# Performance work log

Measured on AMD Instinct MI355X. Metric: run time of the kernel, lower is better.

The kernel has to match this reference:

```python
import jax, jax.numpy as jnp
import numpy as np

RANK = 16
ALPHA = 16.0
SCALING = ALPHA / RANK
N_ADAPTERS = 8


def setup_inputs() -> dict:
    key = jax.random.key(0)
    k_x, k_a, k_b, k_id = jax.random.split(key, 4)
    b, n, d_in, d_out = 8, 1024, 2048, 2048
    x = jax.random.normal(k_x, (b, n, d_in), dtype=jnp.float32)
    A = jax.random.normal(k_a, (N_ADAPTERS, d_out, RANK), dtype=jnp.float32) * 0.02
    B = jax.random.normal(k_b, (N_ADAPTERS, RANK, d_in), dtype=jnp.float32)
    adapter_ids = jax.random.randint(k_id, (b,), 0, N_ADAPTERS, dtype=jnp.int32)
    return {"x": x, "A": A, "B": B, "adapter_ids": adapter_ids}


def reference(x, A, B, adapter_ids):
    # Bx: [b, n, a, r] = einsum over in_features
    Bx = jnp.einsum('bni,ari->bnar', x, B)
    # result: [b, n, a, o]
    result = jnp.einsum('bnar,aor->bnao', Bx, A)
    # per-sample adapter gather: out[b, n, o] = result[b, n, adapter_ids[b], :]
    bidx = jnp.arange(x.shape[0])
    out = result[bidx, :, adapter_ids, :]  # [b, n, o]
    return out * SCALING  # dropout p=0.0 is identity
```

## Files before the change

kernel.cpp:

```cpp
#include <hip/hip_runtime.h>

#define D_IN   2048
#define D_OUT  2048
#define N_TOK  1024
#define N_B    8
#define RANK   16
#define TPB    8

__device__ __forceinline__ float dot4(float4 a, float4 b) {
    return a.x * b.x + a.y * b.y + a.z * b.z + a.w * b.w;
}

template <int CTRL>
__device__ __forceinline__ float dpp_add(float v) {
    int s = __builtin_amdgcn_update_dpp(0, __float_as_int(v), CTRL, 0xF, 0xF, true);
    return v + __int_as_float(s);
}

__device__ __forceinline__ float wave_sum(float v) {
    v = dpp_add<0xB1>(v);
    v = dpp_add<0x4E>(v);
    v = dpp_add<0x124>(v);
    v = dpp_add<0x128>(v);
    v += __shfl_xor(v, 16, 64);
    v += __shfl_xor(v, 32, 64);
    return v;
}

__global__ __launch_bounds__(256, 2)
void lora_fused_v4(const float* __restrict__ x,
                   const float* __restrict__ A,
                   const float* __restrict__ B,
                   const int* __restrict__ ids,
                   float* __restrict__ out) {
    __shared__ __align__(16) float bxs[TPB][RANK];

    const int b    = blockIdx.y;
    const int tok0 = blockIdx.x * TPB;
    const int aid  = ids[b];
    const int tid  = threadIdx.x;
    const int wave = tid >> 6;
    const int lane = tid & 63;

    const float* __restrict__ xb = x + ((size_t)b * N_TOK + tok0 + wave * 2) * D_IN;
    const float* __restrict__ Ba = B + (size_t)aid * RANK * D_IN;
    const float* __restrict__ Aa = A + (size_t)aid * D_OUT * RANK;
    float* __restrict__ ob = out + ((size_t)b * N_TOK + tok0) * D_OUT;

    float acc0[RANK], acc1[RANK];
    #pragma unroll
    for (int r = 0; r < RANK; ++r) { acc0[r] = 0.f; acc1[r] = 0.f; }

    #pragma unroll
    for (int chunk = 0; chunk < 8; ++chunk) {
        const int ib = chunk * 256 + lane * 4;
        const float4 xv0 = *reinterpret_cast<const float4*>(&xb[ib]);
        const float4 xv1 = *reinterpret_cast<const float4*>(&xb[D_IN + ib]);
        #pragma unroll
        for (int g = 0; g < 2; ++g) {
            float4 Bv[8];
            #pragma unroll
            for (int r = 0; r < 8; ++r)
                Bv[r] = *reinterpret_cast<const float4*>(&Ba[(size_t)(g * 8 + r) * D_IN + ib]);
            #pragma unroll
            for (int r = 0; r < 8; ++r) {
                acc0[g * 8 + r] += dot4(xv0, Bv[r]);
                acc1[g * 8 + r] += dot4(xv1, Bv[r]);
            }
        }
    }

    #pragma unroll
    for (int r = 0; r < RANK; ++r) {
        acc0[r] = wave_sum(acc0[r]);
        acc1[r] = wave_sum(acc1[r]);
    }

    if (lane == 0) {
        const int t0 = wave * 2;
        *reinterpret_cast<float4*>(&bxs[t0][0])      = make_float4(acc0[0],  acc0[1],  acc0[2],  acc0[3]);
        *reinterpret_cast<float4*>(&bxs[t0][4])      = make_float4(acc0[4],  acc0[5],  acc0[6],  acc0[7]);
        *reinterpret_cast<float4*>(&bxs[t0][8])      = make_float4(acc0[8],  acc0[9],  acc0[10], acc0[11]);
        *reinterpret_cast<float4*>(&bxs[t0][12])     = make_float4(acc0[12], acc0[13], acc0[14], acc0[15]);
        *reinterpret_cast<float4*>(&bxs[t0 + 1][0])  = make_float4(acc1[0],  acc1[1],  acc1[2],  acc1[3]);
        *reinterpret_cast<float4*>(&bxs[t0 + 1][4])  = make_float4(acc1[4],  acc1[5],  acc1[6],  acc1[7]);
        *reinterpret_cast<float4*>(&bxs[t0 + 1][8])  = make_float4(acc1[8],  acc1[9],  acc1[10], acc1[11]);
        *reinterpret_cast<float4*>(&bxs[t0 + 1][12]) = make_float4(acc1[12], acc1[13], acc1[14], acc1[15]);
    }
    __syncthreads();

    #pragma unroll
    for (int half = 0; half < 2; ++half) {
        const int o0 = half * 1024 + tid * 4;
        float4 Ar[4][4];
        #pragma unroll
        for (int j = 0; j < 4; ++j)
            #pragma unroll
            for (int q = 0; q < 4; ++q)
                Ar[j][q] = *reinterpret_cast<const float4*>(&Aa[(size_t)(o0 + j) * RANK + q * 4]);

        #pragma unroll
        for (int t = 0; t < TPB; ++t) {
            const float4 p0 = *reinterpret_cast<const float4*>(&bxs[t][0]);
            const float4 p1 = *reinterpret_cast<const float4*>(&bxs[t][4]);
            const float4 p2 = *reinterpret_cast<const float4*>(&bxs[t][8]);
            const float4 p3 = *reinterpret_cast<const float4*>(&bxs[t][12]);
            float4 res;
            res.x = dot4(Ar[0][0], p0) + dot4(Ar[0][1], p1) + dot4(Ar[0][2], p2) + dot4(Ar[0][3], p3);
            res.y = dot4(Ar[1][0], p0) + dot4(Ar[1][1], p1) + dot4(Ar[1][2], p2) + dot4(Ar[1][3], p3);
            res.z = dot4(Ar[2][0], p0) + dot4(Ar[2][1], p1) + dot4(Ar[2][2], p2) + dot4(Ar[2][3], p3);
            res.w = dot4(Ar[3][0], p0) + dot4(Ar[3][1], p1) + dot4(Ar[3][2], p2) + dot4(Ar[3][3], p3);
            *reinterpret_cast<float4*>(&ob[(size_t)t * D_OUT + o0]) = res;
        }
    }
}

extern "C" void kernel_launch(void* const* d_in, const int* in_sizes, int n_in,
                              void* d_out, int out_size, void* d_ws, size_t ws_size,
                              hipStream_t stream) {
    const float* x   = (const float*)d_in[0];
    const float* A   = (const float*)d_in[1];
    const float* B   = (const float*)d_in[2];
    const int*   ids = (const int*)d_in[3];
    float* out = (float*)d_out;

    dim3 grid(N_TOK / TPB, N_B);
    lora_fused_v4<<<grid, 256, 0, stream>>>(x, A, B, ids, out);
}
```

Baseline: 148.5 us.

## Split LoRA into split-K Bx kernel and separate output projection kernel

Replaces the fused single kernel with two launches. The first computes partial Bx products, with the input dimension split in two, and writes them to a workspace buffer. The second sums the two partials and applies the A projection, split across two output halves per block. This raises the number of blocks for both phases and shrinks per-thread register pressure, at the cost of an extra launch and a global-memory round trip for the small intermediate.

```diff
diff --git a/kernel.cpp b/kernel.cpp
--- a/kernel.cpp
+++ b/kernel.cpp
@@ -5,10 +5,15 @@
 #define N_TOK  1024
 #define N_B    8
 #define RANK   16
-#define TPB    8
+#define KSPLIT 2
+#define KHALF  (D_IN / KSPLIT)
 
 __device__ __forceinline__ float dot4(float4 a, float4 b) {
     return a.x * b.x + a.y * b.y + a.z * b.z + a.w * b.w;
+}
+
+__device__ __forceinline__ float4 f4add(float4 a, float4 b) {
+    return make_float4(a.x + b.x, a.y + b.y, a.z + b.z, a.w + b.w);
 }
 
 template <int CTRL>
@@ -27,45 +32,42 @@
     return v;
 }
 
+
 __global__ __launch_bounds__(256, 2)
-void lora_fused_v4(const float* __restrict__ x,
-                   const float* __restrict__ A,
-                   const float* __restrict__ B,
-                   const int* __restrict__ ids,
-                   float* __restrict__ out) {
-    __shared__ __align__(16) float bxs[TPB][RANK];
+void lora_bx(const float* __restrict__ x,
+             const float* __restrict__ B,
+             const int* __restrict__ ids,
+             float* __restrict__ W) {
+    const int tile = blockIdx.x;
+    const int ks   = blockIdx.y;
+    const int b    = blockIdx.z;
+    const int aid  = ids[b];
+    const int wave = (int)(threadIdx.x >> 6);
+    const int lane = (int)(threadIdx.x & 63);
+    const int t0   = tile * 8 + wave * 2;
 
-    const int b    = blockIdx.y;
-    const int tok0 = blockIdx.x * TPB;
-    const int aid  = ids[b];
-    const int tid  = threadIdx.x;
-    const int wave = tid >> 6;
-    const int lane = tid & 63;
-
-    const float* __restrict__ xb = x + ((size_t)b * N_TOK + tok0 + wave * 2) * D_IN;
-    const float* __restrict__ Ba = B + (size_t)aid * RANK * D_IN;
-    const float* __restrict__ Aa = A + (size_t)aid * D_OUT * RANK;
-    float* __restrict__ ob = out + ((size_t)b * N_TOK + tok0) * D_OUT;
+    const float* __restrict__ xb = x + ((size_t)b * N_TOK + t0) * D_IN + ks * KHALF;
+    const float* __restrict__ Ba = B + (size_t)aid * RANK * D_IN + ks * KHALF;
 
     float acc0[RANK], acc1[RANK];
     #pragma unroll
     for (int r = 0; r < RANK; ++r) { acc0[r] = 0.f; acc1[r] = 0.f; }
 
     #pragma unroll
-    for (int chunk = 0; chunk < 8; ++chunk) {
+    for (int chunk = 0; chunk < KHALF / 256; ++chunk) {
         const int ib = chunk * 256 + lane * 4;
         const float4 xv0 = *reinterpret_cast<const float4*>(&xb[ib]);
         const float4 xv1 = *reinterpret_cast<const float4*>(&xb[D_IN + ib]);
         #pragma unroll
-        for (int g = 0; g < 2; ++g) {
-            float4 Bv[8];
+        for (int g = 0; g < 4; ++g) {
+            float4 Bv[4];
             #pragma unroll
-            for (int r = 0; r < 8; ++r)
-                Bv[r] = *reinterpret_cast<const float4*>(&Ba[(size_t)(g * 8 + r) * D_IN + ib]);
+            for (int r = 0; r < 4; ++r)
+                Bv[r] = *reinterpret_cast<const float4*>(&Ba[(size_t)(g * 4 + r) * D_IN + ib]);
             #pragma unroll
-            for (int r = 0; r < 8; ++r) {
-                acc0[g * 8 + r] += dot4(xv0, Bv[r]);
-                acc1[g * 8 + r] += dot4(xv1, Bv[r]);
+            for (int r = 0; r < 4; ++r) {
+                acc0[g * 4 + r] += dot4(xv0, Bv[r]);
+                acc1[g * 4 + r] += dot4(xv1, Bv[r]);
             }
         }
     }
@@ -77,41 +79,57 @@
     }
 
     if (lane == 0) {
-        const int t0 = wave * 2;
-        *reinterpret_cast<float4*>(&bxs[t0][0])      = make_float4(acc0[0],  acc0[1],  acc0[2],  acc0[3]);
-        *reinterpret_cast<float4*>(&bxs[t0][4])      = make_float4(acc0[4],  acc0[5],  acc0[6],  acc0[7]);
-        *reinterpret_cast<float4*>(&bxs[t0][8])      = make_float4(acc0[8],  acc0[9],  acc0[10], acc0[11]);
-        *reinterpret_cast<float4*>(&bxs[t0][12])     = make_float4(acc0[12], acc0[13], acc0[14], acc0[15]);
-        *reinterpret_cast<float4*>(&bxs[t0 + 1][0])  = make_float4(acc1[0],  acc1[1],  acc1[2],  acc1[3]);
-        *reinterpret_cast<float4*>(&bxs[t0 + 1][4])  = make_float4(acc1[4],  acc1[5],  acc1[6],  acc1[7]);
-        *reinterpret_cast<float4*>(&bxs[t0 + 1][8])  = make_float4(acc1[8],  acc1[9],  acc1[10], acc1[11]);
-        *reinterpret_cast<float4*>(&bxs[t0 + 1][12]) = make_float4(acc1[12], acc1[13], acc1[14], acc1[15]);
+        float* Wp = W + (((size_t)ks * N_B + b) * N_TOK + t0) * RANK;
+        *reinterpret_cast<float4*>(&Wp[0])         = make_float4(acc0[0],  acc0[1],  acc0[2],  acc0[3]);
+        *reinterpret_cast<float4*>(&Wp[4])         = make_float4(acc0[4],  acc0[5],  acc0[6],  acc0[7]);
+        *reinterpret_cast<float4*>(&Wp[8])         = make_float4(acc0[8],  acc0[9],  acc0[10], acc0[11]);
+        *reinterpret_cast<float4*>(&Wp[12])        = make_float4(acc0[12], acc0[13], acc0[14], acc0[15]);
+        *reinterpret_cast<float4*>(&Wp[RANK + 0])  = make_float4(acc1[0],  acc1[1],  acc1[2],  acc1[3]);
+        *reinterpret_cast<float4*>(&Wp[RANK + 4])  = make_float4(acc1[4],  acc1[5],  acc1[6],  acc1[7]);
+        *reinterpret_cast<float4*>(&Wp[RANK + 8])  = make_float4(acc1[8],  acc1[9],  acc1[10], acc1[11]);
+        *reinterpret_cast<float4*>(&Wp[RANK + 12]) = make_float4(acc1[12], acc1[13], acc1[14], acc1[15]);
     }
-    __syncthreads();
+}
+
+__global__ __launch_bounds__(256, 2)
+void lora_out(const float* __restrict__ A,
+              const int* __restrict__ ids,
+              const float* __restrict__ W,
+              float* __restrict__ out) {
+    const int tile = blockIdx.x;
+    const int half = blockIdx.y;
+    const int b    = blockIdx.z;
+    const int aid  = ids[b];
+    const int o0   = half * 1024 + (int)threadIdx.x * 4;
+
+    const float* __restrict__ Aa  = A + (size_t)aid * D_OUT * RANK;
+    const float* __restrict__ Wb0 = W + ((size_t)b * N_TOK + tile * 8) * RANK;
+    const float* __restrict__ Wb1 = W + (((size_t)N_B + b) * N_TOK + tile * 8) * RANK;
+    float* __restrict__ ob = out + ((size_t)b * N_TOK + tile * 8) * D_OUT;
+
+    float4 Ar[4][4];
+    #pragma unroll
+    for (int j = 0; j < 4; ++j)
+        #pragma unroll
+        for (int q = 0; q < 4; ++q)
+            Ar[j][q] = *reinterpret_cast<const float4*>(&Aa[(size_t)(o0 + j) * RANK + q * 4]);
 
     #pragma unroll
-    for (int half = 0; half < 2; ++half) {
-        const int o0 = half * 1024 + tid * 4;
-        float4 Ar[4][4];
-        #pragma unroll
-        for (int j = 0; j < 4; ++j)
-            #pragma unroll
-            for (int q = 0; q < 4; ++q)
-                Ar[j][q] = *reinterpret_cast<const float4*>(&Aa[(size_t)(o0 + j) * RANK + q * 4]);
-
-        #pragma unroll
-        for (int t = 0; t < TPB; ++t) {
-            const float4 p0 = *reinterpret_cast<const float4*>(&bxs[t][0]);
-            const float4 p1 = *reinterpret_cast<const float4*>(&bxs[t][4]);
-            const float4 p2 = *reinterpret_cast<const float4*>(&bxs[t][8]);
-            const float4 p3 = *reinterpret_cast<const float4*>(&bxs[t][12]);
-            float4 res;
-            res.x = dot4(Ar[0][0], p0) + dot4(Ar[0][1], p1) + dot4(Ar[0][2], p2) + dot4(Ar[0][3], p3);
-            res.y = dot4(Ar[1][0], p0) + dot4(Ar[1][1], p1) + dot4(Ar[1][2], p2) + dot4(Ar[1][3], p3);
-            res.z = dot4(Ar[2][0], p0) + dot4(Ar[2][1], p1) + dot4(Ar[2][2], p2) + dot4(Ar[2][3], p3);
-            res.w = dot4(Ar[3][0], p0) + dot4(Ar[3][1], p1) + dot4(Ar[3][2], p2) + dot4(Ar[3][3], p3);
-            *reinterpret_cast<float4*>(&ob[(size_t)t * D_OUT + o0]) = res;
-        }
+    for (int t = 0; t < 8; ++t) {
+        const float4 p0 = f4add(*reinterpret_cast<const float4*>(&Wb0[t * RANK + 0]),
+                                *reinterpret_cast<const float4*>(&Wb1[t * RANK + 0]));
+        const float4 p1 = f4add(*reinterpret_cast<const float4*>(&Wb0[t * RANK + 4]),
+                                *reinterpret_cast<const float4*>(&Wb1[t * RANK + 4]));
+        const float4 p2 = f4add(*reinterpret_cast<const float4*>(&Wb0[t * RANK + 8]),
+                                *reinterpret_cast<const float4*>(&Wb1[t * RANK + 8]));
+        const float4 p3 = f4add(*reinterpret_cast<const float4*>(&Wb0[t * RANK + 12]),
+                                *reinterpret_cast<const float4*>(&Wb1[t * RANK + 12]));
+        float4 res;
+        res.x = dot4(Ar[0][0], p0) + dot4(Ar[0][1], p1) + dot4(Ar[0][2], p2) + dot4(Ar[0][3], p3);
+        res.y = dot4(Ar[1][0], p0) + dot4(Ar[1][1], p1) + dot4(Ar[1][2], p2) + dot4(Ar[1][3], p3);
+        res.z = dot4(Ar[2][0], p0) + dot4(Ar[2][1], p1) + dot4(Ar[2][2], p2) + dot4(Ar[2][3], p3);
+        res.w = dot4(Ar[3][0], p0) + dot4(Ar[3][1], p1) + dot4(Ar[3][2], p2) + dot4(Ar[3][3], p3);
+        *reinterpret_cast<float4*>(&ob[(size_t)t * D_OUT + o0]) = res;
     }
 }
 
@@ -123,7 +141,11 @@
     const float* B   = (const float*)d_in[2];
     const int*   ids = (const int*)d_in[3];
     float* out = (float*)d_out;
+    float* W   = (float*)d_ws;
 
-    dim3 grid(N_TOK / TPB, N_B);
-    lora_fused_v4<<<grid, 256, 0, stream>>>(x, A, B, ids, out);
+    dim3 g1(N_TOK / 8, KSPLIT, N_B);
+    lora_bx<<<g1, 256, 0, stream>>>(x, B, ids, W);
+
+    dim3 g2(N_TOK / 8, 2, N_B);
+    lora_out<<<g2, 256, 0, stream>>>(A, ids, W, out);
 }
```

Result: slower. 158.4 us (+6.6%).

## Split LoRA into split-K Bx kernel and separate output projection kernel

Applied to the files above, without the earlier changes.

Replaces the single fused kernel with two kernels. The first computes Bx with a split-K over the input dimension: each 64-thread block stages a 64x64 x tile in XOR-swizzled shared memory, each thread owns one token with B read as broadcast loads, and per-split partials go to workspace. The second kernel sums the 16 partials and applies the A projection, now spread over a grid that also splits output halves. The aim is to drop the per-token cross-lane wave reductions and add parallelism, at the cost of a workspace round-trip, an extra launch, and uncoalesced per-lane B access patterns.

```diff
diff --git a/kernel.cpp b/kernel.cpp
--- a/kernel.cpp
+++ b/kernel.cpp
@@ -5,113 +5,130 @@
 #define N_TOK  1024
 #define N_B    8
 #define RANK   16
-#define TPB    8
+#define KS     16
+#define ICH    (D_IN / KS)
 
 __device__ __forceinline__ float dot4(float4 a, float4 b) {
     return a.x * b.x + a.y * b.y + a.z * b.z + a.w * b.w;
 }
 
-template <int CTRL>
-__device__ __forceinline__ float dpp_add(float v) {
-    int s = __builtin_amdgcn_update_dpp(0, __float_as_int(v), CTRL, 0xF, 0xF, true);
-    return v + __int_as_float(s);
-}
+__global__ __launch_bounds__(64)
+void lora_bx_v6(const float* __restrict__ x,
+                const float* __restrict__ B,
+                const int* __restrict__ ids,
+                float* __restrict__ W) {
+    __shared__ __align__(16) float xs[64 * 64];
 
-__device__ __forceinline__ float wave_sum(float v) {
-    v = dpp_add<0xB1>(v);
-    v = dpp_add<0x4E>(v);
-    v = dpp_add<0x124>(v);
-    v = dpp_add<0x128>(v);
-    v += __shfl_xor(v, 16, 64);
-    v += __shfl_xor(v, 32, 64);
-    return v;
-}
+    const int tile = blockIdx.x;
+    const int ks   = blockIdx.y;
+    const int b    = blockIdx.z;
+    const int aid  = ids[b];
+    const int l    = (int)threadIdx.x;
 
-__global__ __launch_bounds__(256, 2)
-void lora_fused_v4(const float* __restrict__ x,
-                   const float* __restrict__ A,
-                   const float* __restrict__ B,
-                   const int* __restrict__ ids,
-                   float* __restrict__ out) {
-    __shared__ __align__(16) float bxs[TPB][RANK];
+    const float* __restrict__ xb = x + ((size_t)b * N_TOK + tile * 64) * D_IN + ks * ICH;
+    const float* __restrict__ Bq = B + (size_t)aid * RANK * D_IN + ks * ICH;
 
-    const int b    = blockIdx.y;
-    const int tok0 = blockIdx.x * TPB;
-    const int aid  = ids[b];
-    const int tid  = threadIdx.x;
-    const int wave = tid >> 6;
-    const int lane = tid & 63;
-
-    const float* __restrict__ xb = x + ((size_t)b * N_TOK + tok0 + wave * 2) * D_IN;
-    const float* __restrict__ Ba = B + (size_t)aid * RANK * D_IN;
-    const float* __restrict__ Aa = A + (size_t)aid * D_OUT * RANK;
-    float* __restrict__ ob = out + ((size_t)b * N_TOK + tok0) * D_OUT;
-
-    float acc0[RANK], acc1[RANK];
+    float acc[RANK];
     #pragma unroll
-    for (int r = 0; r < RANK; ++r) { acc0[r] = 0.f; acc1[r] = 0.f; }
+    for (int r = 0; r < RANK; ++r) acc[r] = 0.f;
 
     #pragma unroll
-    for (int chunk = 0; chunk < 8; ++chunk) {
-        const int ib = chunk * 256 + lane * 4;
-        const float4 xv0 = *reinterpret_cast<const float4*>(&xb[ib]);
-        const float4 xv1 = *reinterpret_cast<const float4*>(&xb[D_IN + ib]);
+    for (int c = 0; c < 2; ++c) {
+        const float* xc = xb + c * 64;
+        const float* Bc = Bq + c * 64;
+
+        __syncthreads();
         #pragma unroll
-        for (int g = 0; g < 2; ++g) {
-            float4 Bv[8];
+        for (int h = 0; h < 2; ++h) {
+            float4 st[8];
             #pragma unroll
-            for (int r = 0; r < 8; ++r)
-                Bv[r] = *reinterpret_cast<const float4*>(&Ba[(size_t)(g * 8 + r) * D_IN + ib]);
+            for (int kk = 0; kk < 8; ++kk) {
+                const int k   = h * 8 + kk;
+                const int row = k * 4 + (l >> 4);
+                const int seg = l & 15;
+                st[kk] = *reinterpret_cast<const float4*>(&xc[(size_t)row * D_IN + seg * 4]);
+            }
             #pragma unroll
-            for (int r = 0; r < 8; ++r) {
-                acc0[g * 8 + r] += dot4(xv0, Bv[r]);
-                acc1[g * 8 + r] += dot4(xv1, Bv[r]);
+            for (int kk = 0; kk < 8; ++kk) {
+                const int k   = h * 8 + kk;
+                const int row = k * 4 + (l >> 4);
+                const int v   = (l & 15) ^ (row & 15);
+                *reinterpret_cast<float4*>(&xs[row * 64 + v * 4]) = st[kk];
+            }
+        }
+        __syncthreads();
+
+        #pragma unroll
+        for (int j = 0; j < 16; ++j) {
+            const int v = j ^ (l & 15);
+            const float4 xv = *reinterpret_cast<const float4*>(&xs[l * 64 + v * 4]);
+            #pragma unroll
+            for (int r = 0; r < RANK; ++r) {
+                const float4 Bv = *reinterpret_cast<const float4*>(&Bc[(size_t)r * D_IN + j * 4]);
+                acc[r] += dot4(xv, Bv);
             }
         }
     }
 
-    #pragma unroll
-    for (int r = 0; r < RANK; ++r) {
-        acc0[r] = wave_sum(acc0[r]);
-        acc1[r] = wave_sum(acc1[r]);
-    }
+    float* Wp = W + (((size_t)ks * N_B + b) * N_TOK + tile * 64 + l) * RANK;
+    *reinterpret_cast<float4*>(&Wp[0])  = make_float4(acc[0],  acc[1],  acc[2],  acc[3]);
+    *reinterpret_cast<float4*>(&Wp[4])  = make_float4(acc[4],  acc[5],  acc[6],  acc[7]);
+    *reinterpret_cast<float4*>(&Wp[8])  = make_float4(acc[8],  acc[9],  acc[10], acc[11]);
+    *reinterpret_cast<float4*>(&Wp[12]) = make_float4(acc[12], acc[13], acc[14], acc[15]);
+}
 
-    if (lane == 0) {
-        const int t0 = wave * 2;
-        *reinterpret_cast<float4*>(&bxs[t0][0])      = make_float4(acc0[0],  acc0[1],  acc0[2],  acc0[3]);
-        *reinterpret_cast<float4*>(&bxs[t0][4])      = make_float4(acc0[4],  acc0[5],  acc0[6],  acc0[7]);
-        *reinterpret_cast<float4*>(&bxs[t0][8])      = make_float4(acc0[8],  acc0[9],  acc0[10], acc0[11]);
-        *reinterpret_cast<float4*>(&bxs[t0][12])     = make_float4(acc0[12], acc0[13], acc0[14], acc0[15]);
-        *reinterpret_cast<float4*>(&bxs[t0 + 1][0])  = make_float4(acc1[0],  acc1[1],  acc1[2],  acc1[3]);
-        *reinterpret_cast<float4*>(&bxs[t0 + 1][4])  = make_float4(acc1[4],  acc1[5],  acc1[6],  acc1[7]);
-        *reinterpret_cast<float4*>(&bxs[t0 + 1][8])  = make_float4(acc1[8],  acc1[9],  acc1[10], acc1[11]);
-        *reinterpret_cast<float4*>(&bxs[t0 + 1][12]) = make_float4(acc1[12], acc1[13], acc1[14], acc1[15]);
+__global__ __launch_bounds__(256, 2)
+void lora_out_v6(const float* __restrict__ A,
+                 const int* __restrict__ ids,
+                 const float* __restrict__ W,
+                 float* __restrict__ out) {
+    __shared__ __align__(16) float bxs[8][RANK];
+
+    const int tile = blockIdx.x;
+    const int half = blockIdx.y;
+    const int b    = blockIdx.z;
+    const int aid  = ids[b];
+    const int tid  = (int)threadIdx.x;
+
+    if (tid < 128) {
+        const int t = tid >> 4, r = tid & 15;
+        const size_t base = ((size_t)b * N_TOK + tile * 8 + t) * RANK + r;
+        const size_t sstr = (size_t)N_B * N_TOK * RANK;
+        float s0 = 0.f, s1 = 0.f, s2 = 0.f, s3 = 0.f;
+        #pragma unroll
+        for (int s = 0; s < KS; s += 4) {
+            s0 += W[(s + 0) * sstr + base];
+            s1 += W[(s + 1) * sstr + base];
+            s2 += W[(s + 2) * sstr + base];
+            s3 += W[(s + 3) * sstr + base];
+        }
+        bxs[t][r] = (s0 + s1) + (s2 + s3);
     }
     __syncthreads();
 
+    const int o0 = half * 1024 + tid * 4;
+    const float* __restrict__ Aa = A + (size_t)aid * D_OUT * RANK;
+    float* __restrict__ ob = out + ((size_t)b * N_TOK + tile * 8) * D_OUT;
+
+    float4 Ar[4][4];
     #pragma unroll
-    for (int half = 0; half < 2; ++half) {
-        const int o0 = half * 1024 + tid * 4;
-        float4 Ar[4][4];
+    for (int j = 0; j < 4; ++j)
         #pragma unroll
-        for (int j = 0; j < 4; ++j)
-            #pragma unroll
-            for (int q = 0; q < 4; ++q)
-                Ar[j][q] = *reinterpret_cast<const float4*>(&Aa[(size_t)(o0 + j) * RANK + q * 4]);
+        for (int q = 0; q < 4; ++q)
+            Ar[j][q] = *reinterpret_cast<const float4*>(&Aa[(size_t)(o0 + j) * RANK + q * 4]);
 
-        #pragma unroll
-        for (int t = 0; t < TPB; ++t) {
-            const float4 p0 = *reinterpret_cast<const float4*>(&bxs[t][0]);
-            const float4 p1 = *reinterpret_cast<const float4*>(&bxs[t][4]);
-            const float4 p2 = *reinterpret_cast<const float4*>(&bxs[t][8]);
-            const float4 p3 = *reinterpret_cast<const float4*>(&bxs[t][12]);
-            float4 res;
-            res.x = dot4(Ar[0][0], p0) + dot4(Ar[0][1], p1) + dot4(Ar[0][2], p2) + dot4(Ar[0][3], p3);
-            res.y = dot4(Ar[1][0], p0) + dot4(Ar[1][1], p1) + dot4(Ar[1][2], p2) + dot4(Ar[1][3], p3);
-            res.z = dot4(Ar[2][0], p0) + dot4(Ar[2][1], p1) + dot4(Ar[2][2], p2) + dot4(Ar[2][3], p3);
-            res.w = dot4(Ar[3][0], p0) + dot4(Ar[3][1], p1) + dot4(Ar[3][2], p2) + dot4(Ar[3][3], p3);
-            *reinterpret_cast<float4*>(&ob[(size_t)t * D_OUT + o0]) = res;
-        }
+    #pragma unroll
+    for (int t = 0; t < 8; ++t) {
+        const float4 p0 = *reinterpret_cast<const float4*>(&bxs[t][0]);
+        const float4 p1 = *reinterpret_cast<const float4*>(&bxs[t][4]);
+        const float4 p2 = *reinterpret_cast<const float4*>(&bxs[t][8]);
+        const float4 p3 = *reinterpret_cast<const float4*>(&bxs[t][12]);
+        float4 res;
+        res.x = dot4(Ar[0][0], p0) + dot4(Ar[0][1], p1) + dot4(Ar[0][2], p2) + dot4(Ar[0][3], p3);
+        res.y = dot4(Ar[1][0], p0) + dot4(Ar[1][1], p1) + dot4(Ar[1][2], p2) + dot4(Ar[1][3], p3);
+        res.z = dot4(Ar[2][0], p0) + dot4(Ar[2][1], p1) + dot4(Ar[2][2], p2) + dot4(Ar[2][3], p3);
+        res.w = dot4(Ar[3][0], p0) + dot4(Ar[3][1], p1) + dot4(Ar[3][2], p2) + dot4(Ar[3][3], p3);
+        *reinterpret_cast<float4*>(&ob[(size_t)t * D_OUT + o0]) = res;
     }
 }
 
@@ -123,7 +140,11 @@
     const float* B   = (const float*)d_in[2];
     const int*   ids = (const int*)d_in[3];
     float* out = (float*)d_out;
+    float* W   = (float*)d_ws;
 
-    dim3 grid(N_TOK / TPB, N_B);
-    lora_fused_v4<<<grid, 256, 0, stream>>>(x, A, B, ids, out);
+    dim3 g1(N_TOK / 64, KS, N_B);
+    lora_bx_v6<<<g1, 64, 0, stream>>>(x, B, ids, W);
+
+    dim3 g2(N_TOK / 8, 2, N_B);
+    lora_out_v6<<<g2, 256, 0, stream>>>(A, ids, W, out);
 }
```

New measurement: 210.7 us. 1.42x slower.
